# Optimization experiments

Hardware: AMD Instinct MI355X
Metric: run time of the kernel (lower is better)

## Reference

```python
import jax, jax.numpy as jnp
import numpy as np

N, E, B = 10000, 160000, 4096
DIN, H, C, HID, HEU = 768, 4, 256, 256, 6

def _gelu(x):
    return jax.nn.gelu(x, approximate=False)

def setup_inputs() -> dict:
    key = jax.random.key(0)
    ks = jax.random.split(key, 30)
    s = 0.02
    inp = {
        'semantic_embeddings': jax.random.normal(ks[0], (B, 2 * DIN), jnp.float32),
        'graph_x': jax.random.normal(ks[1], (N, DIN), jnp.float32),
        'graph_edge_index': jax.random.randint(ks[2], (2, E), 0, N, dtype=jnp.int32),
        'graph_edge_weight': jax.random.uniform(ks[3], (E, 1), jnp.float32),
        'heuristic_features': jax.random.uniform(ks[4], (B, HEU), jnp.float32),
        'node_indices': jax.random.randint(ks[5], (B,), 0, N, dtype=jnp.int32),
        # semantic_proj: Linear(1536,256) GELU Linear(256,256)
        'sem_w1': jax.random.normal(ks[6], (HID, 2 * DIN)) * s,
        'sem_b1': jnp.zeros((HID,), jnp.float32),
        'sem_w2': jax.random.normal(ks[7], (HID, HID)) * s,
        'sem_b2': jnp.zeros((HID,), jnp.float32),
        # GATConv(768 -> 256, heads=4, concat, edge_dim=1)
        'lin_w': jax.random.normal(ks[8], (H * C, DIN)) * s,
        'lin_edge_w': jax.random.normal(ks[9], (H * C, 1)) * s,
        'att_src': jax.random.normal(ks[10], (1, H, C)) * s,
        'att_dst': jax.random.normal(ks[11], (1, H, C)) * s,
        'att_edge': jax.random.normal(ks[12], (1, H, C)) * s,
        'gat_bias': jnp.zeros((H * C,), jnp.float32),
        # structural_proj: Linear(1024,256) GELU
        'struct_w': jax.random.normal(ks[13], (HID, H * C)) * s,
        'struct_b': jnp.zeros((HID,), jnp.float32),
        # HierarchicalResidualFusion
        'gate_w': jax.random.normal(ks[14], (HID, 2 * HID)) * s,
        'gate_b': jnp.zeros((HID,), jnp.float32),
        'heur_w': jax.random.normal(ks[15], (HID, HEU)) * s,
        'heur_b': jnp.zeros((HID,), jnp.float32),
        'hw': jnp.asarray(0.7, jnp.float32),
        'sw1': jax.random.normal(ks[16], (HID, HID)) * s,
        'sb1': jnp.zeros((HID,), jnp.float32),
        'sw2': jax.random.normal(ks[17], (1, HID)) * s,
        'sb2': jnp.zeros((1,), jnp.float32),
    }
    return inp

def reference(semantic_embeddings, graph_x, graph_edge_index, graph_edge_weight,
              heuristic_features, node_indices,
              sem_w1, sem_b1, sem_w2, sem_b2,
              lin_w, lin_edge_w, att_src, att_dst, att_edge, gat_bias,
              struct_w, struct_b,
              gate_w, gate_b, heur_w, heur_b, hw, sw1, sb1, sw2, sb2):
    # --- semantic projection (dropout = identity at eval) ---
    h = _gelu(semantic_embeddings @ sem_w1.T + sem_b1)
    h_sem = h @ sem_w2.T + sem_b2  # [B, HID]

    # --- GATConv with edge_dim=1, add_self_loops (edge_attr fill = mean) ---
    Nn = graph_x.shape[0]
    src = jnp.concatenate([graph_edge_index[0], jnp.arange(Nn, dtype=graph_edge_index.dtype)])
    dst = jnp.concatenate([graph_edge_index[1], jnp.arange(Nn, dtype=graph_edge_index.dtype)])
    ea = jnp.concatenate([graph_edge_weight,
                          jnp.broadcast_to(graph_edge_weight.mean(0, keepdims=True), (Nn, 1))], axis=0)
    x_proj = (graph_x @ lin_w.T).reshape(Nn, H, C)          # [N,H,C]
    a_src_n = (x_proj * att_src).sum(-1)                     # [N,H]
    a_dst_n = (x_proj * att_dst).sum(-1)                     # [N,H]
    e_proj = (ea @ lin_edge_w.T).reshape(-1, H, C)           # [E+N,H,C]
    alpha = a_src_n[src] + a_dst_n[dst] + (e_proj * att_edge).sum(-1)  # [E+N,H]
    alpha = jax.nn.leaky_relu(alpha, 0.2)
    amax = jax.ops.segment_max(alpha, dst, num_segments=Nn)
    expa = jnp.exp(alpha - amax[dst])
    denom = jax.ops.segment_sum(expa, dst, num_segments=Nn)
    coef = expa / denom[dst]                                 # softmax per dst node/head
    msg = x_proj[src] * coef[:, :, None]                     # [E+N,H,C]
    out = jax.ops.segment_sum(msg, dst, num_segments=Nn).reshape(Nn, H * C) + gat_bias
    h_graph = jax.nn.elu(out)

    # --- structural projection on selected nodes ---
    h_struct = _gelu(h_graph[node_indices] @ struct_w.T + struct_b)  # [B,HID]

    # --- hierarchical residual fusion ---
    h_heur = _gelu(heuristic_features @ heur_w.T + heur_b)
    g = jax.nn.sigmoid(jnp.concatenate([h_sem, h_struct], axis=-1) @ gate_w.T + gate_b)
    h_learned = g * h_sem + (1.0 - g) * h_struct
    h_fused = hw * h_heur + (1.0 - hw) * h_learned
    scores = (_gelu(h_fused @ sw1.T + sb1) @ sw2.T + sb2).squeeze(-1)  # [B]
    return scores
```

## Files before the change

kernel.cpp:

```cpp
#include <hip/hip_runtime.h>
#include <math.h>

#define DEV __device__ __forceinline__

typedef __attribute__((ext_vector_type(8))) short bf16x8;
typedef __attribute__((ext_vector_type(4))) float f32x4;

DEV float gelu_f(float x) { return 0.5f * x * (1.f + erff(x * 0.70710678118654752440f)); }

DEV unsigned short f2bf(float f) {
    unsigned u = __float_as_uint(f);
    u += 0x7FFF + ((u >> 16) & 1);
    return (unsigned short)(u >> 16);
}
DEV float bf2f(unsigned short h) { return __uint_as_float(((unsigned)h) << 16); }

DEV void gload_lds16(const void* g, void* l) {
    __builtin_amdgcn_global_load_lds((const __attribute__((address_space(1))) void*)g,
                                     (__attribute__((address_space(3))) void*)l, 16, 0, 0);
}

template<int FM, int FN, int WR, int WC, int EPI, int GATHER, int ASRC, int OUT>
DEV void gemm_body(char* ldsbase, int swz,
                   const unsigned short* __restrict__ Ah, const float* __restrict__ Af,
                   const int* __restrict__ gidx,
                   const unsigned short* __restrict__ Wh, const float* __restrict__ bias,
                   float* __restrict__ C, unsigned short* __restrict__ Ch,
                   int ldsp, int coff,
                   const float* __restrict__ fs_hsem, const float* __restrict__ fs_hstruct,
                   const float* __restrict__ fs_heur, const float* __restrict__ fs_heurw,
                   const float* __restrict__ fs_heurb, const float* __restrict__ fs_hw,
                   int M, int N, int K, int nbx)
{
    constexpr int BK = 64;
    constexpr int BM = WR * FM * 16, BN = WC * FN * 16;
    constexpr int NW = WR * WC;
    unsigned short* sAh = (unsigned short*)ldsbase;
    unsigned short* sWh = (unsigned short*)(ldsbase + BM * BK * 2);

    const int tid = threadIdx.x;
    const int lane = tid & 63;
    const int wid = tid >> 6;
    const int wr = wid / WC, wc = wid % WC;

    const int bx = swz % nbx, by = swz / nbx;
    const int row0 = by * BM;
    const int col0 = bx * BN;

    f32x4 acc[FM][FN];
#pragma unroll
    for (int i = 0; i < FM; i++)
#pragma unroll
        for (int j = 0; j < FN; j++) acc[i][j] = (f32x4){0.f, 0.f, 0.f, 0.f};

    const int srow = lane >> 3;
    const int sslot = lane & 7;

    for (int k0 = 0; k0 < K; k0 += BK) {
#pragma unroll
        for (int c = 0; c < BM / 8 / NW; c++) {
            int call = c * NW + wid;
            int r = call * 8 + srow;
            int gr = row0 + r;
            gr = gr < M ? gr : M - 1;
            if (ASRC == 0) {
                if (GATHER) gr = gidx[gr];
                int b = (sslot ^ (r & 7)) << 4;
                gload_lds16((const char*)(Ah + (size_t)gr * K + k0) + b, (char*)sAh + call * 1024);
            } else {
                const float* sp = Af + (size_t)gr * K + k0 + sslot * 8;
                float vv[8];
                *(float4*)&vv[0] = *(const float4*)sp;
                *(float4*)&vv[4] = *(const float4*)(sp + 4);
                union { bf16x8 v; unsigned short u[8]; } ph;
#pragma unroll
                for (int q = 0; q < 8; q++) ph.u[q] = f2bf(vv[q]);
                int b = (sslot ^ (r & 7)) << 4;
                *(bf16x8*)((char*)sAh + r * 128 + b) = ph.v;
            }
        }
#pragma unroll
        for (int c = 0; c < BN / 8 / NW; c++) {
            int call = c * NW + wid;
            int r = call * 8 + srow;
            int gr = col0 + r;
            int b = (sslot ^ (r & 7)) << 4;
            gload_lds16((const char*)(Wh + (size_t)gr * K + k0) + b, (char*)sWh + call * 1024);
        }
        __syncthreads();

        const int fr = lane & 15, kq = lane >> 4;
#pragma unroll
        for (int ks = 0; ks < 2; ks++) {
            bf16x8 ah[FM], bh[FN];
#pragma unroll
            for (int i = 0; i < FM; i++) {
                int r = wr * FM * 16 + i * 16 + fr;
                int b = ((ks * 4 + kq) ^ (r & 7)) << 4;
                ah[i] = *(const bf16x8*)((const char*)sAh + r * 128 + b);
            }
#pragma unroll
            for (int j = 0; j < FN; j++) {
                int r = wc * FN * 16 + j * 16 + fr;
                int b = ((ks * 4 + kq) ^ (r & 7)) << 4;
                bh[j] = *(const bf16x8*)((const char*)sWh + r * 128 + b);
            }
#pragma unroll
            for (int i = 0; i < FM; i++)
#pragma unroll
                for (int j = 0; j < FN; j++)
                    acc[i][j] = __builtin_amdgcn_mfma_f32_16x16x32_bf16(ah[i], bh[j], acc[i][j], 0, 0, 0);
        }
        __syncthreads();
    }

    const int fr = lane & 15;
    const int r0 = (lane >> 4) * 4;
#pragma unroll
    for (int i = 0; i < FM; i++) {
#pragma unroll
        for (int jj = 0; jj < 4; jj++) {
            int gr = row0 + wr * FM * 16 + i * 16 + r0 + jj;
            if (gr >= M) continue;
            float sacc = 0.f;
#pragma unroll
            for (int j = 0; j < FN; j++) {
                int gc = col0 + wc * FN * 16 + j * 16 + fr;
                float v = acc[i][j][jj] + (bias ? bias[gc] : 0.f);
                if (EPI == 1) v = gelu_f(v);
                else if (EPI == 3) {
                    float g = 1.f / (1.f + expf(-v));
                    float hh = fs_heurb[gc];
#pragma unroll
                    for (int q = 0; q < 6; q++) hh = fmaf(fs_heur[gr * 6 + q], fs_heurw[gc * 6 + q], hh);
                    hh = gelu_f(hh);
                    float hl = g * fs_hsem[(size_t)gr * 256 + gc] + (1.f - g) * fs_hstruct[(size_t)gr * 256 + gc];
                    float hwv = fs_hw[0];
                    v = hwv * hh + (1.f - hwv) * hl;
                }
                if (OUT == 0 || OUT == 2) C[(size_t)gr * N + gc] = v;
                if (OUT == 2 || OUT == 3) Ch[(size_t)gr * ldsp + coff + gc] = f2bf(v);
                if (OUT == 4) sacc = fmaf(v, fs_hsem[gc], sacc);
            }
            if (OUT == 4) {
                sacc += __shfl_xor(sacc, 1);
                sacc += __shfl_xor(sacc, 2);
                sacc += __shfl_xor(sacc, 4);
                sacc += __shfl_xor(sacc, 8);
                if ((lane & 15) == 0) atomicAdd(&C[gr], sacc);
            }
        }
    }
}

DEV int xcd_swz(int bid, int nwg) {
    return ((nwg & 7) == 0) ? (bid & 7) * (nwg >> 3) + (bid >> 3) : bid;
}

template<int FM, int FN, int WR, int WC, int EPI, int GATHER, int ASRC, int OUT>
__global__ __launch_bounds__(WR* WC * 64)
void mgemm_k(const unsigned short* __restrict__ Ah, const float* __restrict__ Af,
             const int* __restrict__ gidx,
             const unsigned short* __restrict__ Wh, const float* __restrict__ bias,
             float* __restrict__ C, unsigned short* __restrict__ Ch,
             int ldsp, int coff,
             const float* __restrict__ fs_hsem, const float* __restrict__ fs_hstruct,
             const float* __restrict__ fs_heur, const float* __restrict__ fs_heurw,
             const float* __restrict__ fs_heurb, const float* __restrict__ fs_hw,
             int M, int N, int K, int nbx)
{
    constexpr int BM = WR * FM * 16, BN = WC * FN * 16;
    __shared__ alignas(16) char lds[(BM + BN) * 64 * 2];
    int swz = xcd_swz(blockIdx.x, gridDim.x);
    gemm_body<FM, FN, WR, WC, EPI, GATHER, ASRC, OUT>(
        lds, swz, Ah, Af, gidx, Wh, bias, C, Ch, ldsp, coff,
        fs_hsem, fs_hstruct, fs_heur, fs_heurw, fs_heurb, fs_hw, M, N, K, nbx);
}

DEV void gat_agg_body(char* shm, int d,
                      const int* __restrict__ ei, const float* __restrict__ ew,
                      const float* __restrict__ scal, const float* __restrict__ a_src,
                      const float* __restrict__ a_dst,
                      const int* __restrict__ count, const int* __restrict__ offs_end,
                      const int* __restrict__ eid, const unsigned short* __restrict__ xpb,
                      const float* __restrict__ gat_bias,
                      unsigned short* __restrict__ aggh, int E)
{
    int* srcs   = (int*)shm;
    float* al   = (float*)(shm + 1024);
    float* mrun = (float*)(shm + 5120);
    float* drun = (float*)(shm + 5136);
    float* scale = (float*)(shm + 5152);
    int c = count[d];
    int start = offs_end[d] - c;
    int tid = threadIdx.x;
    if (tid < 4) { mrun[tid] = -1e30f; drun[tid] = 0.f; }
    float4 acc = make_float4(0.f, 0.f, 0.f, 0.f);
    const int h = tid >> 6;
    const int x = tid * 4;
    const float adst0 = a_dst[d * 4 + 0], adst1 = a_dst[d * 4 + 1],
                adst2 = a_dst[d * 4 + 2], adst3 = a_dst[d * 4 + 3];

    for (int cb = 0; cb < c; cb += 256) {
        int cc = min(256, c - cb);
        __syncthreads();
        for (int t = tid; t < cc * 4; t += 256) {
            int j = t >> 2, hh = t & 3;
            int e = eid[start + cb + j];
            int s; float ea;
            if (e < E) { s = ei[e]; ea = ew[e]; }
            else       { s = e - E; ea = scal[0] / (float)E; }
            float ad = hh == 0 ? adst0 : hh == 1 ? adst1 : hh == 2 ? adst2 : adst3;
            float a = a_src[s * 4 + hh] + ad + ea * scal[1 + hh];
            a = a > 0.f ? a : 0.2f * a;
            al[j * 4 + hh] = a;
            if (hh == 0) srcs[j] = s;
        }
        __syncthreads();
        if (tid < 4) {
            float m = -1e30f;
            for (int j = 0; j < cc; j++) m = fmaxf(m, al[j * 4 + tid]);
            float nm = fmaxf(mrun[tid], m);
            float sc = expf(mrun[tid] - nm);
            scale[tid] = sc;
            drun[tid] *= sc;
            mrun[tid] = nm;
        }
        __syncthreads();
        for (int t = tid; t < cc * 4; t += 256) {
            int j = t >> 2, hh = t & 3;
            al[j * 4 + hh] = expf(al[j * 4 + hh] - mrun[hh]);
        }
        __syncthreads();
        if (tid < 4) {
            float s = 0.f;
            for (int j = 0; j < cc; j++) s += al[j * 4 + tid];
            drun[tid] += s;
        }
        float sc = scale[h];
        acc.x *= sc; acc.y *= sc; acc.z *= sc; acc.w *= sc;
        for (int j = 0; j < cc; j++) {
            float w = al[j * 4 + h];
            ushort4 vv = *(const ushort4*)(xpb + (size_t)srcs[j] * 1024 + x);
            acc.x = fmaf(w, bf2f(vv.x), acc.x);
            acc.y = fmaf(w, bf2f(vv.y), acc.y);
            acc.z = fmaf(w, bf2f(vv.z), acc.z);
            acc.w = fmaf(w, bf2f(vv.w), acc.w);
        }
    }
    __syncthreads();
    float dn = drun[h];
    float4 gb = *(const float4*)(gat_bias + x);
    float t0 = acc.x / dn + gb.x, t1 = acc.y / dn + gb.y,
          t2 = acc.z / dn + gb.z, t3 = acc.w / dn + gb.w;
    t0 = t0 > 0.f ? t0 : expf(t0) - 1.f;
    t1 = t1 > 0.f ? t1 : expf(t1) - 1.f;
    t2 = t2 > 0.f ? t2 : expf(t2) - 1.f;
    t3 = t3 > 0.f ? t3 : expf(t3) - 1.f;
    ushort4 hh;
    hh.x = f2bf(t0); hh.y = f2bf(t1); hh.z = f2bf(t2); hh.w = f2bf(t3);
    *(ushort4*)(aggh + (size_t)d * 1024 + x) = hh;
}

__global__ __launch_bounds__(256)
void dualA_k(const unsigned short* __restrict__ gxh, const unsigned short* __restrict__ linw_h,
             unsigned short* __restrict__ xpb, int Nn, int HC, int DIN, int nbx_x, int nxp,
             const float* __restrict__ sem, const unsigned short* __restrict__ sw1w_h,
             const float* __restrict__ sem_b1, unsigned short* __restrict__ s1h,
             int B, int nbh, int nh1,
             const int* __restrict__ ei, int* __restrict__ offs, int* __restrict__ eid, int E)
{
    __shared__ alignas(16) char lds[32768];
    int bid = blockIdx.x;
    if (bid < nxp) {
        int swz = xcd_swz(bid, nxp);
        gemm_body<4, 4, 2, 2, 0, 0, 0, 3>(
            lds, swz, gxh, nullptr, nullptr, linw_h, nullptr,
            nullptr, xpb, HC, 0, nullptr, nullptr, nullptr, nullptr, nullptr, nullptr,
            Nn, HC, DIN, nbx_x);
    } else if (bid < nxp + nh1) {
        int swz = xcd_swz(bid - nxp, nh1);
        gemm_body<1, 2, 2, 2, 1, 0, 1, 3>(
            lds, swz, nullptr, sem, nullptr, sw1w_h, sem_b1,
            nullptr, s1h, 256, 0, nullptr, nullptr, nullptr, nullptr, nullptr, nullptr,
            B, 256, 2 * DIN, nbh);
    } else {
        int e = (bid - nxp - nh1) * 256 + threadIdx.x;
        if (e < E + Nn) {
            int d = (e < E) ? ei[E + e] : e - E;
            int p = atomicAdd(&offs[d], 1);
            eid[p] = e;
        }
    }
}

__global__ __launch_bounds__(256)
void dualC_k(int Nn, int nh1,
             const int* __restrict__ ei, const float* __restrict__ ew,
             const float* __restrict__ scal, const float* __restrict__ a_src,
             const float* __restrict__ a_dst, const int* __restrict__ needed,
             const int* __restrict__ count, const int* __restrict__ offs_end,
             const int* __restrict__ eid, const unsigned short* __restrict__ xpb,
             const float* __restrict__ gat_bias,
             unsigned short* __restrict__ aggh, int E,
             const unsigned short* __restrict__ s1h,
             const unsigned short* __restrict__ sw2w_h,
             const float* __restrict__ sem_b2, float* __restrict__ h_sem,
             unsigned short* __restrict__ gAh,
             int B, int nbh)
{
    __shared__ alignas(16) char lds[12288];
    int bid = blockIdx.x;
    if (bid < Nn) {
        if (!needed[bid]) return;
        gat_agg_body(lds, bid, ei, ew, scal, a_src, a_dst, count, offs_end, eid,
                     xpb, gat_bias, aggh, E);
    } else {
        int swz = xcd_swz(bid - Nn, nh1);
        gemm_body<1, 2, 2, 2, 0, 0, 0, 2>(
            lds, swz, s1h, nullptr, nullptr, sw2w_h, sem_b2,
            h_sem, gAh, 512, 0, nullptr, nullptr, nullptr, nullptr, nullptr, nullptr,
            B, 256, 256, nbh);
    }
}


__global__ void init_k(int* count, int* needed, float* scal, int Nn,
                       const float* __restrict__ lin_w, const float* __restrict__ att_src,
                       const float* __restrict__ att_dst,
                       float* __restrict__ wsrc, float* __restrict__ wdst,
                       const float* __restrict__ lew, const float* __restrict__ ae, int ZB,
                       float* __restrict__ out, const float* __restrict__ sb2, int B,
                       int* __restrict__ cursor)
{
    int b = blockIdx.x;
    if (b < ZB) {
        int i = b * 256 + threadIdx.x;
        if (i < Nn) { count[i] = 0; needed[i] = 0; }
        if (i < B) out[i] = sb2[0];
        if (i == 0) { scal[0] = 0.f; cursor[0] = 0; }
        return;
    }
    if (b < ZB + 12) {
        int gid = (b - ZB) * 256 + threadIdx.x;
        if (gid >= 4 * 768) return;
        int h = gid / 768, k = gid % 768;
        float ss = 0.f, sd = 0.f;
        for (int c = 0; c < 256; c++) {
            float w = lin_w[(size_t)(h * 256 + c) * 768 + k];
            ss = fmaf(w, att_src[h * 256 + c], ss);
            sd = fmaf(w, att_dst[h * 256 + c], sd);
        }
        wsrc[k * 4 + h] = ss;
        wdst[k * 4 + h] = sd;
        return;
    }
    int w = threadIdx.x / 64, lane = threadIdx.x % 64;
    float c = 0.f;
    for (int cc = lane; cc < 256; cc += 64) c += lew[w * 256 + cc] * ae[w * 256 + cc];
    for (int off = 32; off; off >>= 1) c += __shfl_down(c, off);
    if (lane == 0) scal[1 + w] = c;
}

__global__ __launch_bounds__(256)
void mega1_k(int Nn, int nW, int nCnt, int nMark, int nEw,
             const float* __restrict__ gx, unsigned short* __restrict__ gxh,
             const float* __restrict__ wsrc, const float* __restrict__ wdst,
             float* __restrict__ a_src, float* __restrict__ a_dst,
             const float* s0, unsigned short* h0, int e0,
             const float* s1, unsigned short* h1, int e1,
             const float* s2, unsigned short* h2, int e2,
             const float* s3, unsigned short* h3, int e3,
             const float* s4, unsigned short* h4, int e4,
             const float* s5, unsigned short* h5, int e5,
             const int* __restrict__ ei, int* __restrict__ count, int E,
             const int* __restrict__ nidx, int* __restrict__ needed, int B,
             const float* __restrict__ ew, float* __restrict__ scal)
{
    __shared__ float sh[256];
    int b = blockIdx.x;
    int t = threadIdx.x;

    if (b < Nn) {
        int node = b;
        float acc[8] = {0.f, 0.f, 0.f, 0.f, 0.f, 0.f, 0.f, 0.f};
        if (t < 192) {
            float4 v = ((const float4*)(gx + (size_t)node * 768))[t];
            ushort4 h;
            h.x = f2bf(v.x); h.y = f2bf(v.y); h.z = f2bf(v.z); h.w = f2bf(v.w);
            ((ushort4*)(gxh + (size_t)node * 768))[t] = h;
            float vv[4] = {v.x, v.y, v.z, v.w};
#pragma unroll
            for (int q = 0; q < 4; q++) {
                int k = t * 4 + q;
                float4 wsv = *(const float4*)(wsrc + k * 4);
                float4 wdv = *(const float4*)(wdst + k * 4);
                acc[0] = fmaf(vv[q], wsv.x, acc[0]); acc[1] = fmaf(vv[q], wsv.y, acc[1]);
                acc[2] = fmaf(vv[q], wsv.z, acc[2]); acc[3] = fmaf(vv[q], wsv.w, acc[3]);
                acc[4] = fmaf(vv[q], wdv.x, acc[4]); acc[5] = fmaf(vv[q], wdv.y, acc[5]);
                acc[6] = fmaf(vv[q], wdv.z, acc[6]); acc[7] = fmaf(vv[q], wdv.w, acc[7]);
            }
        }
#pragma unroll
        for (int i = 0; i < 8; i++)
            for (int off = 32; off; off >>= 1) acc[i] += __shfl_down(acc[i], off);
        int lane = t & 63, wid = t >> 6;
        if (lane == 0)
#pragma unroll
            for (int i = 0; i < 8; i++) sh[wid * 8 + i] = acc[i];
        __syncthreads();
        if (t < 8) {
            float s = sh[t] + sh[8 + t] + sh[16 + t] + sh[24 + t];
            if (t < 4) a_src[node * 4 + t] = s;
            else       a_dst[node * 4 + (t - 4)] = s;
        }
        return;
    }
    b -= Nn;
    if (b < nW) {
        int i = b * 256 + t;
        const float* s; unsigned short* h; int j;
        if (i < e0)      { s = s0; h = h0; j = i; }
        else if (i < e1) { s = s1; h = h1; j = i - e0; }
        else if (i < e2) { s = s2; h = h2; j = i - e1; }
        else if (i < e3) { s = s3; h = h3; j = i - e2; }
        else if (i < e4) { s = s4; h = h4; j = i - e3; }
        else if (i < e5) { s = s5; h = h5; j = i - e4; }
        else return;
        float4 v = ((const float4*)s)[j];
        ushort4 hh;
        hh.x = f2bf(v.x); hh.y = f2bf(v.y); hh.z = f2bf(v.z); hh.w = f2bf(v.w);
        ((ushort4*)h)[j] = hh;
        return;
    }
    b -= nW;
    if (b < nCnt) {
        int e = b * 256 + t;
        if (e >= E + Nn) return;
        int d = (e < E) ? ei[E + e] : e - E;
        atomicAdd(&count[d], 1);
        return;
    }
    b -= nCnt;
    if (b < nMark) {
        int gid = b * 256 + t;
        if (gid < B) needed[nidx[gid]] = 1;
        return;
    }
    b -= nMark;
    float s = 0.f;
    for (int i = b * 256 + t; i < E; i += nEw * 256) s += ew[i];
    sh[t] = s;
    __syncthreads();
    for (int off = 128; off; off >>= 1) {
        if (t < off) sh[t] += sh[t + off];
        __syncthreads();
    }
    if (t == 0) atomicAdd(&scal[0], sh[0]);
}

__global__ void alloc_k(const int* __restrict__ count, int* __restrict__ offs,
                        int* __restrict__ cursor, int Nn)
{
    int d = blockIdx.x * 256 + threadIdx.x;
    if (d < Nn) offs[d] = atomicAdd(cursor, count[d]);
}


extern "C" void kernel_launch(void* const* d_in, const int* in_sizes, int n_in,
                              void* d_out, int out_size, void* d_ws, size_t ws_size,
                              hipStream_t stream)
{
    const float* sem      = (const float*)d_in[0];
    const float* gx       = (const float*)d_in[1];
    const int*   ei       = (const int*)d_in[2];
    const float* ew       = (const float*)d_in[3];
    const float* heur     = (const float*)d_in[4];
    const int*   nidx     = (const int*)d_in[5];
    const float* sem_w1   = (const float*)d_in[6];
    const float* sem_b1   = (const float*)d_in[7];
    const float* sem_w2   = (const float*)d_in[8];
    const float* sem_b2   = (const float*)d_in[9];
    const float* lin_w    = (const float*)d_in[10];
    const float* lin_edge = (const float*)d_in[11];
    const float* att_src  = (const float*)d_in[12];
    const float* att_dst  = (const float*)d_in[13];
    const float* att_edge = (const float*)d_in[14];
    const float* gat_bias = (const float*)d_in[15];
    const float* struct_w = (const float*)d_in[16];
    const float* struct_b = (const float*)d_in[17];
    const float* gate_w   = (const float*)d_in[18];
    const float* gate_b   = (const float*)d_in[19];
    const float* heur_w   = (const float*)d_in[20];
    const float* heur_b   = (const float*)d_in[21];
    const float* hwp      = (const float*)d_in[22];
    const float* sw1      = (const float*)d_in[23];
    const float* sb1      = (const float*)d_in[24];
    const float* sw2      = (const float*)d_in[25];
    const float* sb2      = (const float*)d_in[26];
    float* out = (float*)d_out;

    const int DIN = 768, HC = 1024, HID = 256;
    const int B  = in_sizes[0] / (2 * DIN);
    const int Nn = in_sizes[1] / DIN;
    const int E  = in_sizes[3];

    float* ws = (float*)d_ws;
    size_t off = 0;
    auto alloc = [&](size_t n) { float* p = ws + off; off += n; return p; };
    auto allocU = [&](size_t nelem) { return (unsigned short*)alloc((nelem + 1) / 2); };

    unsigned short* xpb  = allocU((size_t)Nn * HC);
    unsigned short* aggh = allocU((size_t)Nn * HC);
    float* h_sem    = alloc((size_t)B * HID);
    float* h_struct = alloc((size_t)B * HID);
    unsigned short* s1h = allocU((size_t)B * HID);
    unsigned short* gAh = allocU((size_t)B * 512);
    unsigned short* fuh = allocU((size_t)B * HID);
    float* a_src    = alloc((size_t)Nn * 4);
    float* a_dst    = alloc((size_t)Nn * 4);
    float* wsrc     = alloc((size_t)DIN * 4);
    float* wdst     = alloc((size_t)DIN * 4);
    int* countb     = (int*)alloc((size_t)Nn);
    int* offsb      = (int*)alloc((size_t)Nn);
    int* neededb    = (int*)alloc((size_t)Nn);
    int* eidb       = (int*)alloc((size_t)(E + Nn));
    float* scal     = alloc(8);
    int* cursorb    = (int*)alloc(4);
    unsigned short* linw_h = allocU((size_t)HC * DIN);
    unsigned short* sw1w_h = allocU((size_t)HID * 2 * DIN);
    unsigned short* sw2w_h = allocU((size_t)HID * HID);
    unsigned short* stw_h  = allocU((size_t)HID * HC);
    unsigned short* gaw_h  = allocU((size_t)HID * 512);
    unsigned short* scw_h  = allocU((size_t)HID * HID);
    unsigned short* gxh    = allocU((size_t)Nn * DIN);
    (void)ws_size; (void)n_in; (void)out_size;

    int ZB = (Nn + 255) / 256;
    init_k<<<ZB + 13, 256, 0, stream>>>(countb, neededb, scal, Nn,
                                        lin_w, att_src, att_dst, wsrc, wdst,
                                        lin_edge, att_edge, ZB, out, sb2, B, cursorb);

    int c0 = (HC * DIN) / 4;
    int c1 = c0 + (HID * 2 * DIN) / 4;
    int c2 = c1 + (HID * HID) / 4;
    int c3 = c2 + (HID * HC) / 4;
    int c4 = c3 + (HID * 512) / 4;
    int c5 = c4 + (HID * HID) / 4;
    int nW = (c5 + 255) / 256;
    int tot = E + Nn;
    int nCnt = (tot + 255) / 256;
    int nMark = (B + 255) / 256;
    int nEw = 256;
    mega1_k<<<Nn + nW + nCnt + nMark + nEw, 256, 0, stream>>>(
        Nn, nW, nCnt, nMark, nEw,
        gx, gxh, wsrc, wdst, a_src, a_dst,
        lin_w, linw_h, c0,
        sem_w1, sw1w_h, c1,
        sem_w2, sw2w_h, c2,
        struct_w, stw_h, c3,
        gate_w, gaw_h, c4,
        sw1, scw_h, c5,
        ei, countb, E,
        nidx, neededb, B,
        ew, scal);

    alloc_k<<<(Nn + 255) / 256, 256, 0, stream>>>(countb, offsb, cursorb, Nn);

    const int nbx_x = HC / 128;
    const int nby_x = (Nn + 127) / 128;
    const int nxp = nbx_x * nby_x;
    const int nbh = HID / 64;
    const int nh1 = (B / 32) * nbh;
    const int nF = (tot + 255) / 256;
    dualA_k<<<nxp + nh1 + nF, 256, 0, stream>>>(gxh, linw_h, xpb, Nn, HC, DIN, nbx_x, nxp,
                                                sem, sw1w_h, sem_b1, s1h,
                                                B, nbh, nh1, ei, offsb, eidb, E);

    dualC_k<<<Nn + nh1, 256, 0, stream>>>(Nn, nh1,
                                          ei, ew, scal, a_src, a_dst, neededb, countb, offsb, eidb,
                                          xpb, gat_bias, aggh, E,
                                          s1h, sw2w_h, sem_b2, h_sem, gAh, B, nbh);

    mgemm_k<1, 2, 2, 2, 1, 1, 0, 2><<<nh1, 256, 0, stream>>>(
        aggh, nullptr, nidx, stw_h, struct_b,
        h_struct, gAh, 512, 256, nullptr, nullptr, nullptr, nullptr, nullptr, nullptr,
        B, HID, HC, nbh);

    mgemm_k<1, 2, 2, 2, 3, 0, 0, 3><<<nh1, 256, 0, stream>>>(
        gAh, nullptr, nullptr, gaw_h, gate_b,
        nullptr, fuh, HID, 0, h_sem, h_struct, heur, heur_w, heur_b, hwp,
        B, HID, 512, nbh);

    mgemm_k<1, 2, 2, 2, 1, 0, 0, 4><<<nh1, 256, 0, stream>>>(
        fuh, nullptr, nullptr, scw_h, sb1,
        out, nullptr, 0, 0, sw2, nullptr, nullptr, nullptr, nullptr, nullptr,
        B, HID, HID, nbh);
}
```

Before: 179.0 us.

## Fuse three tail GEMM launches into one persistent kernel with grid barriers

Replaces the three back-to-back small GEMM launches (structural projection, gate fusion, scoring) with one kernel. The stages are separated by atomic-counter grid barriers, with the counter kept in the cursor buffer and zeroed by the init kernel. This removes two kernel launch gaps and their drain/fill bubbles. The trade-off is spin-wait barriers that need all nh1=512 blocks to be co-resident (launch bounds of 2 blocks per CU), which risks deadlock on a smaller device and adds barrier latency.

```diff
diff --git a/kernel.cpp b/kernel.cpp
--- a/kernel.cpp
+++ b/kernel.cpp
@@ -157,24 +157,50 @@
     return ((nwg & 7) == 0) ? (bid & 7) * (nwg >> 3) + (bid >> 3) : bid;
 }
 
-template<int FM, int FN, int WR, int WC, int EPI, int GATHER, int ASRC, int OUT>
-__global__ __launch_bounds__(WR* WC * 64)
-void mgemm_k(const unsigned short* __restrict__ Ah, const float* __restrict__ Af,
-             const int* __restrict__ gidx,
-             const unsigned short* __restrict__ Wh, const float* __restrict__ bias,
-             float* __restrict__ C, unsigned short* __restrict__ Ch,
-             int ldsp, int coff,
-             const float* __restrict__ fs_hsem, const float* __restrict__ fs_hstruct,
-             const float* __restrict__ fs_heur, const float* __restrict__ fs_heurw,
-             const float* __restrict__ fs_heurb, const float* __restrict__ fs_hw,
-             int M, int N, int K, int nbx)
-{
-    constexpr int BM = WR * FM * 16, BN = WC * FN * 16;
-    __shared__ alignas(16) char lds[(BM + BN) * 64 * 2];
-    int swz = xcd_swz(blockIdx.x, gridDim.x);
-    gemm_body<FM, FN, WR, WC, EPI, GATHER, ASRC, OUT>(
-        lds, swz, Ah, Af, gidx, Wh, bias, C, Ch, ldsp, coff,
-        fs_hsem, fs_hstruct, fs_heur, fs_heurw, fs_heurb, fs_hw, M, N, K, nbx);
+DEV void gridbar(int* bar, int target) {
+    __syncthreads();
+    if (threadIdx.x == 0) {
+        __threadfence();
+        atomicAdd(bar, 1);
+        while (atomicAdd(bar, 0) < target) __builtin_amdgcn_s_sleep(2);
+        __threadfence();
+    }
+    __syncthreads();
+}
+
+__global__ __launch_bounds__(256, 2)
+void tail3_k(const unsigned short* __restrict__ aggh, const int* __restrict__ nidx,
+             const unsigned short* __restrict__ stw_h, const float* __restrict__ struct_b,
+             float* __restrict__ h_struct, unsigned short* __restrict__ gAh,
+             const unsigned short* __restrict__ gaw_h, const float* __restrict__ gate_b,
+             const float* __restrict__ h_sem,
+             const float* __restrict__ heur, const float* __restrict__ heur_w,
+             const float* __restrict__ heur_b, const float* __restrict__ hwp,
+             unsigned short* __restrict__ fuh,
+             const unsigned short* __restrict__ scw_h, const float* __restrict__ sb1,
+             const float* __restrict__ sw2, float* __restrict__ out,
+             int B, int HC, int nbh, int* __restrict__ bar)
+{
+    __shared__ alignas(16) char lds[12288];
+    const int nwg = gridDim.x;
+    const int swz = xcd_swz(blockIdx.x, nwg);
+
+    gemm_body<1, 2, 2, 2, 1, 1, 0, 2>(
+        lds, swz, aggh, nullptr, nidx, stw_h, struct_b,
+        h_struct, gAh, 512, 256, nullptr, nullptr, nullptr, nullptr, nullptr, nullptr,
+        B, 256, HC, nbh);
+    gridbar(bar, nwg);
+
+    gemm_body<1, 2, 2, 2, 3, 0, 0, 3>(
+        lds, swz, gAh, nullptr, nullptr, gaw_h, gate_b,
+        nullptr, fuh, 256, 0, h_sem, h_struct, heur, heur_w, heur_b, hwp,
+        B, 256, 512, nbh);
+    gridbar(bar, 2 * nwg);
+
+    gemm_body<1, 2, 2, 2, 1, 0, 0, 4>(
+        lds, swz, fuh, nullptr, nullptr, scw_h, sb1,
+        out, nullptr, 0, 0, sw2, nullptr, nullptr, nullptr, nullptr, nullptr,
+        B, 256, 256, nbh);
 }
 
 DEV void gat_agg_body(char* shm, int d,
@@ -338,7 +364,7 @@
         int i = b * 256 + threadIdx.x;
         if (i < Nn) { count[i] = 0; needed[i] = 0; }
         if (i < B) out[i] = sb2[0];
-        if (i == 0) { scal[0] = 0.f; cursor[0] = 0; }
+        if (i == 0) { scal[0] = 0.f; cursor[0] = 0; cursor[1] = 0; }
         return;
     }
     if (b < ZB + 12) {
@@ -526,7 +552,7 @@
     int* neededb    = (int*)alloc((size_t)Nn);
     int* eidb       = (int*)alloc((size_t)(E + Nn));
     float* scal     = alloc(8);
-    int* cursorb    = (int*)alloc(4);
+    int* cursorb    = (int*)alloc(2);
     unsigned short* linw_h = allocU((size_t)HC * DIN);
     unsigned short* sw1w_h = allocU((size_t)HID * 2 * DIN);
     unsigned short* sw2w_h = allocU((size_t)HID * HID);
@@ -582,18 +608,7 @@
                                           xpb, gat_bias, aggh, E,
                                           s1h, sw2w_h, sem_b2, h_sem, gAh, B, nbh);
 
-    mgemm_k<1, 2, 2, 2, 1, 1, 0, 2><<<nh1, 256, 0, stream>>>(
-        aggh, nullptr, nidx, stw_h, struct_b,
-        h_struct, gAh, 512, 256, nullptr, nullptr, nullptr, nullptr, nullptr, nullptr,
-        B, HID, HC, nbh);
-
-    mgemm_k<1, 2, 2, 2, 3, 0, 0, 3><<<nh1, 256, 0, stream>>>(
-        gAh, nullptr, nullptr, gaw_h, gate_b,
-        nullptr, fuh, HID, 0, h_sem, h_struct, heur, heur_w, heur_b, hwp,
-        B, HID, 512, nbh);
-
-    mgemm_k<1, 2, 2, 2, 1, 0, 0, 4><<<nh1, 256, 0, stream>>>(
-        fuh, nullptr, nullptr, scw_h, sb1,
-        out, nullptr, 0, 0, sw2, nullptr, nullptr, nullptr, nullptr, nullptr,
-        B, HID, HID, nbh);
-}
+    tail3_k<<<nh1, 256, 0, stream>>>(aggh, nidx, stw_h, struct_b, h_struct, gAh,
+                                     gaw_h, gate_b, h_sem, heur, heur_w, heur_b, hwp,
+                                     fuh, scw_h, sb1, sw2, out, B, HC, nbh, cursorb + 1);
+}
```

After: 264.1 us. 1.47x slower.
